# Optimization experiments

Measured on AMD Instinct MI355X. Metric: run time of the kernel, lower is better.

## Reference

```python
import jax, jax.numpy as jnp
import numpy as np

N_NODES = 50000
N_EDGES = 262144
N_OCP = 32768
N_GRAPHS = 64
H = 128          # hidden_size
F_IN = 128       # node feature dim (== H for the stub GNN)
N_LABELS = 10


def _lin(key, fan_in, fan_out):
    return jax.random.normal(key, (fan_in, fan_out), jnp.float32) * (1.0 / float(np.sqrt(fan_in)))


def setup_inputs() -> dict:
    key = jax.random.key(0)
    ks = jax.random.split(key, 16)
    x = jax.random.normal(ks[0], (N_NODES, F_IN), jnp.float32)
    edge_index = jax.random.randint(ks[1], (2, N_EDGES), 0, N_NODES)
    batch_vec = jnp.sort(jax.random.randint(ks[2], (N_NODES,), 0, N_GRAPHS))
    y = jax.random.randint(ks[3], (N_GRAPHS,), 0, N_LABELS)
    params = {
        # stub GNN (get_node_reps): one GCN-style layer
        'W_self': _lin(ks[4], F_IN, H),
        'W_nbr': _lin(ks[5], F_IN, H),
        'b_gnn': jnp.zeros((H,), jnp.float32),
        # edge_action_rep_generator: Linear(2H,4H) ELU Linear(4H,2H) ELU Linear(2H,H)
        'Wr1': _lin(ks[6], 2 * H, 4 * H), 'br1': jnp.zeros((4 * H,), jnp.float32),
        'Wr2': _lin(ks[7], 4 * H, 2 * H), 'br2': jnp.zeros((2 * H,), jnp.float32),
        'Wr3': _lin(ks[8], 2 * H, H),     'br3': jnp.zeros((H,), jnp.float32),
        # edge_action_prob_generator: Linear(H,H) ELU Linear(H,num_labels)
        'Wp1': _lin(ks[9], H, H),         'bp1': jnp.zeros((H,), jnp.float32),
        'Wp2': _lin(ks[10], H, N_LABELS), 'bp2': jnp.zeros((N_LABELS,), jnp.float32),
    }
    return dict(x=x, edge_index=edge_index, batch_vec=batch_vec, y=y, n_ocp=N_OCP, **params)


def reference(x, edge_index, batch_vec, y, n_ocp,
              W_self, W_nbr, b_gnn,
              Wr1, br1, Wr2, br2, Wr3, br3,
              Wp1, bp1, Wp2, bp2):
    N = x.shape[0]
    G = y.shape[0]

    def get_node_reps(ei):
        # stub for self.model.get_node_reps: elu(x @ W_self + A @ (x @ W_nbr))
        msg = x[ei[0]] @ W_nbr                                   # [E', H]
        agg = jax.ops.segment_sum(msg, ei[1], num_segments=N)    # [N, H]
        return jax.nn.elu(x @ W_self + agg + b_gnn)

    ocp_edge_index = edge_index[:, :n_ocp]    # state == True edges
    ava_edge_index = edge_index[:, n_ocp:]    # state == False edges

    ava_node_reps = get_node_reps(edge_index) - get_node_reps(ocp_edge_index)  # [N, H]

    # gather per available edge + concat src/dst reps -> [E_ava, 2H]
    a = jnp.concatenate([ava_node_reps[ava_edge_index[0]],
                         ava_node_reps[ava_edge_index[1]]], axis=1)
    # edge_action_rep_generator
    a = jax.nn.elu(a @ Wr1 + br1)
    a = jax.nn.elu(a @ Wr2 + br2)
    a = a @ Wr3 + br3                                            # [E_ava, H]
    # edge_action_prob_generator
    h = jax.nn.elu(a @ Wp1 + bp1)
    logits = h @ Wp2 + bp2                                       # [E_ava, L]

    seg = batch_vec[ava_edge_index[0]]                           # graph id per ava edge
    y_edge = y[seg]                                              # target label per edge
    sel = jnp.take_along_axis(logits, y_edge[:, None], axis=1)[:, 0]  # gather(1, y)

    # segment-wise softmax over edges of each graph
    mx = jax.ops.segment_max(sel, seg, num_segments=G)
    ex = jnp.exp(sel - mx[seg])
    probs = ex / jax.ops.segment_sum(ex, seg, num_segments=G)[seg]    # [E_ava]

    # scatter_max: per-graph max prob and its argmax edge index
    pmax = jax.ops.segment_max(probs, seg, num_segments=G)            # [G]
    E = probs.shape[0]
    idx = jnp.where(probs == pmax[seg], jnp.arange(E), E)
    added_actions = jax.ops.segment_min(idx, seg, num_segments=G)     # [G]

    return probs, pmax, added_actions
```

## Files before the change

kernel.cpp:

```cpp
#include <hip/hip_runtime.h>

#define NN   50000
#define NNP  50048
#define NE   262144
#define NOCP 32768
#define EAVA (NE - NOCP)
#define NG   64
#define HD   128
#define CAP  48
#define CHNK 32768

typedef _Float16 f16x8 __attribute__((ext_vector_type(8)));
typedef _Float16 f16x2 __attribute__((ext_vector_type(2)));
typedef float f32x4 __attribute__((ext_vector_type(4)));

__device__ __forceinline__ float elu_f(float v) { return v > 0.f ? v : (expf(v) - 1.f); }

__device__ __forceinline__ unsigned fenc(float f) {
  unsigned u = __float_as_uint(f);
  return (u & 0x80000000u) ? ~u : (u | 0x80000000u);
}
__device__ __forceinline__ float fdec(unsigned u) {
  return __uint_as_float((u & 0x80000000u) ? (u & 0x7fffffffu) : ~u);
}

__device__ __forceinline__ void dma16(const void* g, void* l) {
  __builtin_amdgcn_global_load_lds((const __attribute__((address_space(1))) unsigned int*)g,
                                   (__attribute__((address_space(3))) unsigned int*)l,
                                   16, 0, 0);
}

__global__ __launch_bounds__(256) void zero_i(int* __restrict__ p, int n) {
  for (int i = blockIdx.x * 256 + threadIdx.x; i < n; i += gridDim.x * 256) p[i] = 0;
}

__global__ void init_small(unsigned* mx_enc, float* denom, unsigned* pmax_enc, int* amin) {
  int t = threadIdx.x;
  if (t < NG) { mx_enc[t] = 0u; denom[t] = 0.f; pmax_enc[t] = 0u; amin[t] = EAVA; }
}

__global__ __launch_bounds__(256) void zero_tails(_Float16* __restrict__ base) {
  int t = blockIdx.x * 256 + threadIdx.x;
  if (t >= 6 * 768) return;
  int arr = t / 768, off = t % 768;
  f16x8 z = {};
  *(f16x8*)(base + (size_t)arr * NNP * HD + (size_t)NN * HD + (size_t)off * 8) = z;
}

__global__ __launch_bounds__(256) void bucket_kernel(const int* __restrict__ ei,
    int* __restrict__ cnt, int* __restrict__ bucket) {
  int e = blockIdx.x * 256 + threadIdx.x;
  if (e >= NE) return;
  int dst = ei[NE + e];
  int src = ei[e];
  int slot = atomicAdd(&cnt[dst], 1);
  if (slot < CAP)
    bucket[(size_t)dst * CAP + slot] = (int)((unsigned)src | (e < NOCP ? 0x80000000u : 0u));
}

__global__ __launch_bounds__(256) void gather_kernel(const float* __restrict__ x,
    const int* __restrict__ cnt, const int* __restrict__ bucket,
    _Float16* __restrict__ xsah, _Float16* __restrict__ xsal,
    _Float16* __restrict__ xsoh, _Float16* __restrict__ xsol) {
  int n = blockIdx.x * 4 + (threadIdx.x >> 6);
  if (n >= NN) return;
  int lane = threadIdx.x & 63;
  int c = cnt[n];
  if (c > CAP) c = CAP;
  float2 aall = make_float2(0.f, 0.f), aocp = aall;
  const int* bk = bucket + (size_t)n * CAP;
  for (int i0 = 0; i0 < c; i0 += 4) {
    int4 pk = *(const int4*)(bk + i0);
    bool m1 = (i0 + 1 < c), m2 = (i0 + 2 < c), m3 = (i0 + 3 < c);
    int r0 = pk.x & 0x7fffffff;
    int r1 = m1 ? (pk.y & 0x7fffffff) : 0;
    int r2 = m2 ? (pk.z & 0x7fffffff) : 0;
    int r3 = m3 ? (pk.w & 0x7fffffff) : 0;
    float2 v0 = *(const float2*)(x + (size_t)r0 * HD + lane * 2);
    float2 v1 = *(const float2*)(x + (size_t)r1 * HD + lane * 2);
    float2 v2 = *(const float2*)(x + (size_t)r2 * HD + lane * 2);
    float2 v3 = *(const float2*)(x + (size_t)r3 * HD + lane * 2);
    aall.x += v0.x; aall.y += v0.y;
    if (pk.x < 0) { aocp.x += v0.x; aocp.y += v0.y; }
    if (m1) { aall.x += v1.x; aall.y += v1.y; if (pk.y < 0) { aocp.x += v1.x; aocp.y += v1.y; } }
    if (m2) { aall.x += v2.x; aall.y += v2.y; if (pk.z < 0) { aocp.x += v2.x; aocp.y += v2.y; } }
    if (m3) { aall.x += v3.x; aall.y += v3.y; if (pk.w < 0) { aocp.x += v3.x; aocp.y += v3.y; } }
  }
  size_t o = (size_t)n * HD + lane * 2;
  _Float16 h0 = (_Float16)aall.x, h1 = (_Float16)aall.y;
  *(f16x2*)(xsah + o) = (f16x2){h0, h1};
  *(f16x2*)(xsal + o) = (f16x2){(_Float16)(aall.x - (float)h0), (_Float16)(aall.y - (float)h1)};
  _Float16 g0 = (_Float16)aocp.x, g1 = (_Float16)aocp.y;
  *(f16x2*)(xsoh + o) = (f16x2){g0, g1};
  *(f16x2*)(xsol + o) = (f16x2){(_Float16)(aocp.x - (float)g0), (_Float16)(aocp.y - (float)g1)};
}

__global__ __launch_bounds__(256) void split_x(const float* __restrict__ r,
    _Float16* __restrict__ rh, _Float16* __restrict__ rl) {
  int t = blockIdx.x * 256 + threadIdx.x;
  if (t >= NN * HD / 8) return;
  const float4* p = (const float4*)(r + (size_t)t * 8);
  float4 v0 = p[0], v1 = p[1];
  float vv[8] = {v0.x, v0.y, v0.z, v0.w, v1.x, v1.y, v1.z, v1.w};
  f16x8 hv, lv;
#pragma unroll
  for (int j = 0; j < 8; ++j) {
    _Float16 hh = (_Float16)vv[j];
    hv[j] = hh;
    lv[j] = (_Float16)(vv[j] - (float)hh);
  }
  *(f16x8*)(rh + (size_t)t * 8) = hv;
  *(f16x8*)(rl + (size_t)t * 8) = lv;
}

__global__ void pack_w2(const float* __restrict__ Wself, const float* __restrict__ Wnbr,
    _Float16* __restrict__ oh, _Float16* __restrict__ ol) {
  int chunk = blockIdx.x;
  int lane = threadIdx.x;
  int ns = chunk & 7, kt = chunk >> 3;
  int n = ns * 16 + (lane & 15);
  int k0 = kt * 32 + (lane >> 4) * 8;
  f16x8 hv, lv;
#pragma unroll
  for (int j = 0; j < 8; ++j) {
    int k = k0 + j;
    float v = (k < 128) ? Wself[(size_t)k * 128 + n] : Wnbr[(size_t)(k - 128) * 128 + n];
    _Float16 hh = (_Float16)v;
    hv[j] = hh;
    lv[j] = (_Float16)(v - (float)hh);
  }
  *(f16x8*)(oh + (size_t)chunk * 512 + lane * 8) = hv;
  *(f16x8*)(ol + (size_t)chunk * 512 + lane * 8) = lv;
}

__global__ void pack_w(const float* __restrict__ W, int K, int N,
    _Float16* __restrict__ oh, _Float16* __restrict__ ol) {
  int chunk = blockIdx.x;
  int lane = threadIdx.x;
  int NS = N >> 4;
  int ns = chunk % NS, kt = chunk / NS;
  int n = ns * 16 + (lane & 15);
  int k0 = kt * 32 + (lane >> 4) * 8;
  f16x8 hv, lv;
#pragma unroll
  for (int j = 0; j < 8; ++j) {
    float v = W[(size_t)(k0 + j) * N + n];
    _Float16 hh = (_Float16)v;
    hv[j] = hh;
    lv[j] = (_Float16)(v - (float)hh);
  }
  *(f16x8*)(oh + (size_t)chunk * 512 + lane * 8) = hv;
  *(f16x8*)(ol + (size_t)chunk * 512 + lane * 8) = lv;
}

__global__ void w34_kernel(const float* __restrict__ Wr3, const float* __restrict__ Wp1,
    const float* __restrict__ br3, const float* __restrict__ bp1,
    float* __restrict__ W34, float* __restrict__ b34) {
  int i = blockIdx.x, j = threadIdx.x;
  float s = 0.f;
  for (int k = 0; k < 128; ++k) s += Wr3[i * 128 + k] * Wp1[k * 128 + j];
  W34[i * 128 + j] = s;
  if (i == 0) {
    float t = bp1[j];
    for (int k = 0; k < 128; ++k) t += br3[k] * Wp1[k * 128 + j];
    b34[j] = t;
  }
}

template <int KT, int NS_B, int AMODE, int KT_NEXT>
__global__ __launch_bounds__(256) void gemm_ab(
    const _Float16* __restrict__ Ah, const _Float16* __restrict__ Al,
    const int* __restrict__ idx0, const int* __restrict__ idx1,
    const _Float16* __restrict__ Bh, const _Float16* __restrict__ Bl,
    const float* __restrict__ bias,
    _Float16* __restrict__ Oh, _Float16* __restrict__ Ol) {
  __shared__ char smem[49152] __attribute__((aligned(16)));
  float* sC = (float*)smem;

  const int tid = threadIdx.x;
  const int w = tid >> 6, lane = tid & 63;
  const int l16 = lane & 15, g16 = lane >> 4;
  const int bm = blockIdx.x * 128, bn = blockIdx.y * 64;
  const int w2r = w >> 1, w2c = w & 1;
  const int bmT = bm >> 4, bnS = bn >> 4;

  f32x4 acc[4][2];
#pragma unroll
  for (int i = 0; i < 4; ++i)
#pragma unroll
    for (int j = 0; j < 2; ++j) acc[i][j] = (f32x4)0.f;

  int i0a = 0, i0b = 0, i1a = 0, i1b = 0;
  if constexpr (AMODE == 1) {
    int rr0 = bm + w * 32 + l16;
    i0a = idx0[rr0]; i0b = idx0[rr0 + 16];
    i1a = idx1[rr0]; i1b = idx1[rr0 + 16];
  }

  auto STAGE = [&](int kt, int buf) {
    char* base = smem + buf * 24576;
    if constexpr (AMODE == 0) {
#pragma unroll
      for (int s = 0; s < 2; ++s) {
        int msub = w * 2 + s;
        size_t ch = (size_t)(bmT + msub) * KT + kt;
        dma16((const char*)Ah + ch * 1024 + lane * 16, base + msub * 1024);
        dma16((const char*)Al + ch * 1024 + lane * 16, base + 8192 + msub * 1024);
      }
    } else {
      int col = (kt & 3) * 32 + g16 * 8;
      int r0 = (kt < 4) ? i0a : i1a;
      int r1 = (kt < 4) ? i0b : i1b;
      dma16(Ah + (size_t)r0 * HD + col, base + (w * 2) * 1024);
      dma16(Al + (size_t)r0 * HD + col, base + 8192 + (w * 2) * 1024);
      dma16(Ah + (size_t)r1 * HD + col, base + (w * 2 + 1) * 1024);
      dma16(Al + (size_t)r1 * HD + col, base + 8192 + (w * 2 + 1) * 1024);
    }
    size_t chb = (size_t)kt * NS_B + bnS + w;
    dma16((const char*)Bh + chb * 1024 + lane * 16, base + 16384 + w * 1024);
    dma16((const char*)Bl + chb * 1024 + lane * 16, base + 20480 + w * 1024);
  };

  auto COMPUTE = [&](int buf) {
    const _Float16* sAh = (const _Float16*)(smem + buf * 24576);
    const _Float16* sAl = (const _Float16*)(smem + buf * 24576 + 8192);
    const _Float16* sBh = (const _Float16*)(smem + buf * 24576 + 16384);
    const _Float16* sBl = (const _Float16*)(smem + buf * 24576 + 20480);
    f16x8 ah[4], al[4];
#pragma unroll
    for (int mi = 0; mi < 4; ++mi) {
      ah[mi] = *(const f16x8*)(sAh + (w2r * 4 + mi) * 512 + lane * 8);
      al[mi] = *(const f16x8*)(sAl + (w2r * 4 + mi) * 512 + lane * 8);
    }
#pragma unroll
    for (int ni = 0; ni < 2; ++ni) {
      f16x8 bh = *(const f16x8*)(sBh + (w2c * 2 + ni) * 512 + lane * 8);
      f16x8 bl = *(const f16x8*)(sBl + (w2c * 2 + ni) * 512 + lane * 8);
#pragma unroll
      for (int mi = 0; mi < 4; ++mi) {
        acc[mi][ni] = __builtin_amdgcn_mfma_f32_16x16x32_f16(ah[mi], bh, acc[mi][ni], 0, 0, 0);
        acc[mi][ni] = __builtin_amdgcn_mfma_f32_16x16x32_f16(al[mi], bh, acc[mi][ni], 0, 0, 0);
        acc[mi][ni] = __builtin_amdgcn_mfma_f32_16x16x32_f16(ah[mi], bl, acc[mi][ni], 0, 0, 0);
      }
    }
  };

  STAGE(0, 0);
  __builtin_amdgcn_s_waitcnt(0);
  __syncthreads();
  for (int kt = 0; kt < KT; kt += 2) {
    STAGE(kt + 1, 1);
    COMPUTE(0);
    __builtin_amdgcn_s_waitcnt(0);
    __syncthreads();
    if (kt + 2 < KT) STAGE(kt + 2, 0);
    COMPUTE(1);
    __builtin_amdgcn_s_waitcnt(0);
    __syncthreads();
  }

#pragma unroll
  for (int ni = 0; ni < 2; ++ni) {
    int colL = (w2c * 2 + ni) * 16 + l16;
    float bv = bias[bn + colL];
#pragma unroll
    for (int mi = 0; mi < 4; ++mi) {
      int rowb = w2r * 64 + mi * 16 + g16 * 4;
#pragma unroll
      for (int r = 0; r < 4; ++r)
        sC[(rowb + r) * 68 + colL] = elu_f(acc[mi][ni][r] + bv);
    }
  }
  __syncthreads();
  const int bnT32 = bn >> 5;
#pragma unroll
  for (int c = 0; c < 4; ++c) {
    int chunkid = w * 4 + c;
    int msub = chunkid >> 1, ktl = chunkid & 1;
    int m = msub * 16 + l16;
    int cb = ktl * 32 + g16 * 8;
    f16x8 hv, lv;
#pragma unroll
    for (int j = 0; j < 8; ++j) {
      float v = sC[m * 68 + cb + j];
      _Float16 hh = (_Float16)v;
      hv[j] = hh;
      lv[j] = (_Float16)(v - (float)hh);
    }
    size_t gchunk = (size_t)(bmT + msub) * KT_NEXT + (bnT32 + ktl);
    *(f16x8*)((char*)Oh + gchunk * 1024 + lane * 16) = hv;
    *(f16x8*)((char*)Ol + gchunk * 1024 + lane * 16) = lv;
  }
}

__global__ __launch_bounds__(64) void reps_direct(
    const _Float16* __restrict__ xh, const _Float16* __restrict__ xl,
    const _Float16* __restrict__ xsah, const _Float16* __restrict__ xsal,
    const _Float16* __restrict__ xsoh, const _Float16* __restrict__ xsol,
    const _Float16* __restrict__ Wsh, const _Float16* __restrict__ Wsl,
    const float* __restrict__ bias,
    _Float16* __restrict__ Oh, _Float16* __restrict__ Ol) {
  __shared__ float sC[64][68];
  const int lane = threadIdx.x;
  const int mt = blockIdx.x, nt = blockIdx.y;
  const int bm = mt * 64, bn = nt * 64;
  const int l16 = lane & 15, g16 = lane >> 4;

  f32x4 acc1[4][4], acc2[4][4];
#pragma unroll
  for (int i = 0; i < 4; ++i)
#pragma unroll
    for (int j = 0; j < 4; ++j) acc1[i][j] = (f32x4)0.f;

  auto CP3 = [&](f32x4 (*acc)[4], const f16x8* ah, const f16x8* al,
                 const f16x8* bh, const f16x8* bl) {
#pragma unroll
    for (int ni = 0; ni < 4; ++ni)
#pragma unroll
      for (int mi = 0; mi < 4; ++mi) {
        acc[mi][ni] = __builtin_amdgcn_mfma_f32_16x16x32_f16(ah[mi], bh[ni], acc[mi][ni], 0, 0, 0);
        acc[mi][ni] = __builtin_amdgcn_mfma_f32_16x16x32_f16(al[mi], bh[ni], acc[mi][ni], 0, 0, 0);
        acc[mi][ni] = __builtin_amdgcn_mfma_f32_16x16x32_f16(ah[mi], bl[ni], acc[mi][ni], 0, 0, 0);
      }
  };

#pragma unroll
  for (int kt = 0; kt < 4; ++kt) {
    f16x8 ah[4], al[4], bh[4], bl[4];
#pragma unroll
    for (int mi = 0; mi < 4; ++mi) {
      size_t off = (size_t)(bm + mi * 16 + l16) * HD + kt * 32 + g16 * 8;
      ah[mi] = *(const f16x8*)(xh + off);
      al[mi] = *(const f16x8*)(xl + off);
    }
#pragma unroll
    for (int ni = 0; ni < 4; ++ni) {
      size_t ch = (size_t)kt * 8 + nt * 4 + ni;
      bh[ni] = *(const f16x8*)(Wsh + ch * 512 + lane * 8);
      bl[ni] = *(const f16x8*)(Wsl + ch * 512 + lane * 8);
    }
    CP3(acc1, ah, al, bh, bl);
  }
#pragma unroll
  for (int i = 0; i < 4; ++i)
#pragma unroll
    for (int j = 0; j < 4; ++j) acc2[i][j] = acc1[i][j];

#pragma unroll
  for (int kt = 0; kt < 4; ++kt) {
    f16x8 aah[4], aal[4], aoh[4], aol[4], bh[4], bl[4];
#pragma unroll
    for (int mi = 0; mi < 4; ++mi) {
      size_t off = (size_t)(bm + mi * 16 + l16) * HD + kt * 32 + g16 * 8;
      aah[mi] = *(const f16x8*)(xsah + off);
      aal[mi] = *(const f16x8*)(xsal + off);
      aoh[mi] = *(const f16x8*)(xsoh + off);
      aol[mi] = *(const f16x8*)(xsol + off);
    }
#pragma unroll
    for (int ni = 0; ni < 4; ++ni) {
      size_t ch = (size_t)(kt + 4) * 8 + nt * 4 + ni;
      bh[ni] = *(const f16x8*)(Wsh + ch * 512 + lane * 8);
      bl[ni] = *(const f16x8*)(Wsl + ch * 512 + lane * 8);
    }
    CP3(acc1, aah, aal, bh, bl);
    CP3(acc2, aoh, aol, bh, bl);
  }

#pragma unroll
  for (int ni = 0; ni < 4; ++ni) {
    int colL = ni * 16 + l16;
    float bv = bias[bn + colL];
#pragma unroll
    for (int mi = 0; mi < 4; ++mi) {
      int rowb = mi * 16 + g16 * 4;
#pragma unroll
      for (int r = 0; r < 4; ++r)
        sC[rowb + r][colL] = elu_f(acc1[mi][ni][r] + bv) - elu_f(acc2[mi][ni][r] + bv);
    }
  }
  __syncthreads();
#pragma unroll
  for (int c = 0; c < 8; ++c) {
    int msub = c >> 1, ktl = c & 1;
    int m = msub * 16 + l16;
    int cb = ktl * 32 + g16 * 8;
    int grow = bm + m;
    if (grow < NN) {
      f16x8 hv, lv;
#pragma unroll
      for (int j = 0; j < 8; ++j) {
        float v = sC[m][cb + j];
        _Float16 hh = (_Float16)v;
        hv[j] = hh;
        lv[j] = (_Float16)(v - (float)hh);
      }
      *(f16x8*)(Oh + (size_t)grow * HD + bn + cb) = hv;
      *(f16x8*)(Ol + (size_t)grow * HD + bn + cb) = lv;
    }
  }
}

__global__ __launch_bounds__(256) void gemm3_sel(
    const _Float16* __restrict__ Ah, const _Float16* __restrict__ Al,
    const _Float16* __restrict__ Bh, const _Float16* __restrict__ Bl,
    const float* __restrict__ b34,
    const int* __restrict__ ei, const int* __restrict__ batchv, const int* __restrict__ yv,
    const float* __restrict__ Wp2, const float* __restrict__ bp2,
    float* __restrict__ sel, int* __restrict__ seg, int co) {
  __shared__ char smem[49152] __attribute__((aligned(16)));
  const int tid = threadIdx.x;
  const int w = tid >> 6, lane = tid & 63;
  const int l16 = lane & 15, g16 = lane >> 4;
  const int mt = blockIdx.x;

  f32x4 acc[8];
#pragma unroll
  for (int j = 0; j < 8; ++j) acc[j] = (f32x4)0.f;

  auto STAGE = [&](int kt, int buf) {
    char* base = smem + buf * 24576;
    size_t ch = (size_t)(mt * 4 + w) * 8 + kt;
    dma16((const char*)Ah + ch * 1024 + lane * 16, base + w * 1024);
    dma16((const char*)Al + ch * 1024 + lane * 16, base + 4096 + w * 1024);
#pragma unroll
    for (int s = 0; s < 2; ++s) {
      int nsub = w * 2 + s;
      size_t chb = (size_t)kt * 8 + nsub;
      dma16((const char*)Bh + chb * 1024 + lane * 16, base + 8192 + nsub * 1024);
      dma16((const char*)Bl + chb * 1024 + lane * 16, base + 16384 + nsub * 1024);
    }
  };

  auto COMPUTE = [&](int buf) {
    const _Float16* sAh = (const _Float16*)(smem + buf * 24576);
    const _Float16* sAl = (const _Float16*)(smem + buf * 24576 + 4096);
    const _Float16* sBh = (const _Float16*)(smem + buf * 24576 + 8192);
    const _Float16* sBl = (const _Float16*)(smem + buf * 24576 + 16384);
    f16x8 ah = *(const f16x8*)(sAh + w * 512 + lane * 8);
    f16x8 al = *(const f16x8*)(sAl + w * 512 + lane * 8);
#pragma unroll
    for (int ni = 0; ni < 8; ++ni) {
      f16x8 bh = *(const f16x8*)(sBh + ni * 512 + lane * 8);
      f16x8 bl = *(const f16x8*)(sBl + ni * 512 + lane * 8);
      acc[ni] = __builtin_amdgcn_mfma_f32_16x16x32_f16(ah, bh, acc[ni], 0, 0, 0);
      acc[ni] = __builtin_amdgcn_mfma_f32_16x16x32_f16(al, bh, acc[ni], 0, 0, 0);
      acc[ni] = __builtin_amdgcn_mfma_f32_16x16x32_f16(ah, bl, acc[ni], 0, 0, 0);
    }
  };

  STAGE(0, 0);
  __builtin_amdgcn_s_waitcnt(0);
  __syncthreads();
  for (int kt = 0; kt < 8; kt += 2) {
    STAGE(kt + 1, 1);
    COMPUTE(0);
    __builtin_amdgcn_s_waitcnt(0);
    __syncthreads();
    if (kt + 2 < 8) STAGE(kt + 2, 0);
    COMPUTE(1);
    __builtin_amdgcn_s_waitcnt(0);
    __syncthreads();
  }

  float bb[8];
#pragma unroll
  for (int ni = 0; ni < 8; ++ni) bb[ni] = b34[ni * 16 + l16];

#pragma unroll
  for (int rr = 0; rr < 4; ++rr) {
    int row = w * 16 + g16 * 4 + rr;
    int e = co + mt * 64 + row;
    int s = ei[NOCP + e];
    int gg = batchv[s];
    int c = yv[gg];
    float a = 0.f;
#pragma unroll
    for (int ni = 0; ni < 8; ++ni)
      a += elu_f(acc[ni][rr] + bb[ni]) * Wp2[(ni * 16 + l16) * 10 + c];
    a += __shfl_xor(a, 1);
    a += __shfl_xor(a, 2);
    a += __shfl_xor(a, 4);
    a += __shfl_xor(a, 8);
    if (l16 == 0) { sel[e] = a + bp2[c]; seg[e] = gg; }
  }
}

__global__ __launch_bounds__(256) void segmax_sel(const float* __restrict__ sel,
    const int* __restrict__ seg, unsigned* __restrict__ mx_enc) {
  __shared__ unsigned sm[NG];
  int tid = threadIdx.x;
  if (tid < NG) sm[tid] = 0u;
  __syncthreads();
  for (int i = blockIdx.x * blockDim.x + tid; i < EAVA; i += gridDim.x * blockDim.x)
    atomicMax(&sm[seg[i]], fenc(sel[i]));
  __syncthreads();
  if (tid < NG) atomicMax(&mx_enc[tid], sm[tid]);
}

__global__ __launch_bounds__(256) void exden_kernel(const float* __restrict__ sel,
    const int* __restrict__ seg, const unsigned* __restrict__ mx_enc,
    float* __restrict__ denom, float* __restrict__ out_probs) {
  __shared__ float sd[NG];
  __shared__ float smx[NG];
  int tid = threadIdx.x;
  if (tid < NG) { smx[tid] = fdec(mx_enc[tid]); sd[tid] = 0.f; }
  __syncthreads();
  for (int i = blockIdx.x * blockDim.x + tid; i < EAVA; i += gridDim.x * blockDim.x) {
    int g = seg[i];
    float ex = expf(sel[i] - smx[g]);
    out_probs[i] = ex;
    atomicAdd(&sd[g], ex);
  }
  __syncthreads();
  if (tid < NG) atomicAdd(&denom[tid], sd[tid]);
}

__global__ __launch_bounds__(256) void probpmax_kernel(const int* __restrict__ seg,
    const float* __restrict__ denom, float* __restrict__ out_probs,
    unsigned* __restrict__ pmax_enc) {
  __shared__ float sden[NG];
  __shared__ unsigned sp[NG];
  int tid = threadIdx.x;
  if (tid < NG) { sden[tid] = denom[tid]; sp[tid] = 0u; }
  __syncthreads();
  for (int i = blockIdx.x * blockDim.x + tid; i < EAVA; i += gridDim.x * blockDim.x) {
    int g = seg[i];
    float p = out_probs[i] / sden[g];
    out_probs[i] = p;
    atomicMax(&sp[g], fenc(p));
  }
  __syncthreads();
  if (tid < NG) atomicMax(&pmax_enc[tid], sp[tid]);
}

__global__ __launch_bounds__(256) void argmin_kernel(const int* __restrict__ seg,
    const float* __restrict__ out_probs, const unsigned* __restrict__ pmax_enc,
    int* __restrict__ amin) {
  __shared__ float spm[NG];
  __shared__ int sa[NG];
  int tid = threadIdx.x;
  if (tid < NG) { spm[tid] = fdec(pmax_enc[tid]); sa[tid] = EAVA; }
  __syncthreads();
  for (int i = blockIdx.x * blockDim.x + tid; i < EAVA; i += gridDim.x * blockDim.x) {
    int g = seg[i];
    if (out_probs[i] == spm[g]) atomicMin(&sa[g], i);
  }
  __syncthreads();
  if (tid < NG) atomicMin(&amin[tid], sa[tid]);
}

__global__ void finalize_kernel(const unsigned* __restrict__ pmax_enc,
    const int* __restrict__ amin, float* __restrict__ out) {
  int g = threadIdx.x;
  if (g < NG) {
    out[EAVA + g] = fdec(pmax_enc[g]);
    out[EAVA + NG + g] = (float)amin[g];
  }
}

extern "C" void kernel_launch(void* const* d_in, const int* in_sizes, int n_in,
                              void* d_out, int out_size, void* d_ws, size_t ws_size,
                              hipStream_t stream) {
  const float* x      = (const float*)d_in[0];
  const int*   ei     = (const int*)d_in[1];
  const int*   batchv = (const int*)d_in[2];
  const int*   yv     = (const int*)d_in[3];
  const float* Wself = (const float*)d_in[5];
  const float* Wnbr  = (const float*)d_in[6];
  const float* bgnn  = (const float*)d_in[7];
  const float* Wr1   = (const float*)d_in[8];
  const float* br1   = (const float*)d_in[9];
  const float* Wr2   = (const float*)d_in[10];
  const float* br2   = (const float*)d_in[11];
  const float* Wr3   = (const float*)d_in[12];
  const float* br3   = (const float*)d_in[13];
  const float* Wp1   = (const float*)d_in[14];
  const float* bp1   = (const float*)d_in[15];
  const float* Wp2   = (const float*)d_in[16];
  const float* bp2   = (const float*)d_in[17];
  float* out = (float*)d_out;

  char* wp = (char*)d_ws;
  auto alloc = [&](size_t bytes) -> char* {
    char* p = wp;
    wp += (bytes + 255) & ~(size_t)255;
    return p;
  };
  _Float16* xsplit = (_Float16*)alloc((size_t)6 * NNP * HD * 2);
  _Float16* xh   = xsplit + (size_t)0 * NNP * HD;
  _Float16* xl   = xsplit + (size_t)1 * NNP * HD;
  _Float16* xsah = xsplit + (size_t)2 * NNP * HD;
  _Float16* xsal = xsplit + (size_t)3 * NNP * HD;
  _Float16* xsoh = xsplit + (size_t)4 * NNP * HD;
  _Float16* xsol = xsplit + (size_t)5 * NNP * HD;
  _Float16*  reps_h   = (_Float16*)alloc((size_t)NN * HD * 2);
  _Float16*  reps_l   = (_Float16*)alloc((size_t)NN * HD * 2);
  int*       cnt      = (int*)alloc((size_t)NN * 4);
  int*       bucket   = (int*)alloc((size_t)NN * CAP * 4);
  float*     sel      = (float*)alloc((size_t)EAVA * 4);
  int*       seg      = (int*)alloc((size_t)EAVA * 4);
  unsigned*  mx_enc   = (unsigned*)alloc(NG * 4);
  float*     denom    = (float*)alloc(NG * 4);
  unsigned*  pmax_enc = (unsigned*)alloc(NG * 4);
  int*       amin     = (int*)alloc(NG * 4);
  _Float16*  Wsh  = (_Float16*)alloc((size_t)64 * 1024);
  _Float16*  Wsl  = (_Float16*)alloc((size_t)64 * 1024);
  _Float16*  Wr1h = (_Float16*)alloc((size_t)8 * 32 * 1024);
  _Float16*  Wr1l = (_Float16*)alloc((size_t)8 * 32 * 1024);
  _Float16*  Wr2h = (_Float16*)alloc((size_t)16 * 16 * 1024);
  _Float16*  Wr2l = (_Float16*)alloc((size_t)16 * 16 * 1024);
  float*     W34  = (float*)alloc((size_t)256 * 128 * 4);
  float*     b34  = (float*)alloc(128 * 4);
  _Float16*  W34h = (_Float16*)alloc((size_t)8 * 8 * 1024);
  _Float16*  W34l = (_Float16*)alloc((size_t)8 * 8 * 1024);
  _Float16*  b1h = (_Float16*)alloc((size_t)(CHNK / 16) * 16 * 1024);
  _Float16*  b1l = (_Float16*)alloc((size_t)(CHNK / 16) * 16 * 1024);
  _Float16*  b2h = (_Float16*)alloc((size_t)(CHNK / 16) * 8 * 1024);
  _Float16*  b2l = (_Float16*)alloc((size_t)(CHNK / 16) * 8 * 1024);
  (void)ws_size;

  zero_i<<<64, 256, 0, stream>>>(cnt, NN);
  init_small<<<1, 64, 0, stream>>>(mx_enc, denom, pmax_enc, amin);
  zero_tails<<<18, 256, 0, stream>>>(xsplit);
  bucket_kernel<<<NE / 256, 256, 0, stream>>>(ei, cnt, bucket);
  gather_kernel<<<(NN + 3) / 4, 256, 0, stream>>>(x, cnt, bucket, xsah, xsal, xsoh, xsol);
  split_x<<<(NN * HD / 8 + 255) / 256, 256, 0, stream>>>(x, xh, xl);
  pack_w2<<<64, 64, 0, stream>>>(Wself, Wnbr, Wsh, Wsl);
  reps_direct<<<dim3(NNP / 64, 2), 64, 0, stream>>>(xh, xl, xsah, xsal, xsoh, xsol, Wsh, Wsl,
                                                    bgnn, reps_h, reps_l);
  w34_kernel<<<256, 128, 0, stream>>>(Wr3, Wp1, br3, bp1, W34, b34);
  pack_w<<<8 * 32, 64, 0, stream>>>(Wr1, 256, 512, Wr1h, Wr1l);
  pack_w<<<16 * 16, 64, 0, stream>>>(Wr2, 512, 256, Wr2h, Wr2l);
  pack_w<<<8 * 8, 64, 0, stream>>>(W34, 256, 128, W34h, W34l);

  for (int c = 0; c < 7; ++c) {
    int co = c * CHNK;
    gemm_ab<8, 32, 1, 16><<<dim3(CHNK / 128, 8), 256, 0, stream>>>(
        reps_h, reps_l, ei + NOCP + co, ei + NE + NOCP + co, Wr1h, Wr1l, br1, b1h, b1l);
    gemm_ab<16, 16, 0, 8><<<dim3(CHNK / 128, 4), 256, 0, stream>>>(
        b1h, b1l, nullptr, nullptr, Wr2h, Wr2l, br2, b2h, b2l);
    gemm3_sel<<<CHNK / 64, 256, 0, stream>>>(
        b2h, b2l, W34h, W34l, b34, ei, batchv, yv, Wp2, bp2, sel, seg, co);
  }

  segmax_sel<<<112, 256, 0, stream>>>(sel, seg, mx_enc);
  exden_kernel<<<112, 256, 0, stream>>>(sel, seg, mx_enc, denom, out);
  probpmax_kernel<<<112, 256, 0, stream>>>(seg, denom, out, pmax_enc);
  argmin_kernel<<<112, 256, 0, stream>>>(seg, out, pmax_enc, amin);
  finalize_kernel<<<1, 64, 0, stream>>>(pmax_enc, amin, out);
}
```

Baseline: 966.8 us.

## Triple-buffer GEMM LDS staging with partial vmcnt waits and swap grid axes

The GEMM kernels move from a double-buffered loop that drains all loads (waitcnt 0) before every compute step to a three-stage ring buffer. Loads run two k-tiles ahead and the code waits only on the older tile using vmcnt thresholds. The grid axes are also swapped so that blocks sharing the same M rows (the gathered A tiles) launch next to each other, which should improve cache reuse. The trade-off is 72KB of LDS per block instead of 48KB, which can lower occupancy, and the hard-coded vmcnt counts must exactly match the number of loads issued per stage.

```diff
diff --git a/kernel.cpp b/kernel.cpp
--- a/kernel.cpp
+++ b/kernel.cpp
@@ -13,6 +13,10 @@
 typedef _Float16 f16x8 __attribute__((ext_vector_type(8)));
 typedef _Float16 f16x2 __attribute__((ext_vector_type(2)));
 typedef float f32x4 __attribute__((ext_vector_type(4)));
+
+#define WAITVM12() asm volatile("s_waitcnt vmcnt(12)" ::: "memory")
+#define WAITVM6()  asm volatile("s_waitcnt vmcnt(6)" ::: "memory")
+#define WAITVM0()  asm volatile("s_waitcnt vmcnt(0)" ::: "memory")
 
 __device__ __forceinline__ float elu_f(float v) { return v > 0.f ? v : (expf(v) - 1.f); }
 
@@ -174,13 +178,13 @@
     const _Float16* __restrict__ Bh, const _Float16* __restrict__ Bl,
     const float* __restrict__ bias,
     _Float16* __restrict__ Oh, _Float16* __restrict__ Ol) {
-  __shared__ char smem[49152] __attribute__((aligned(16)));
+  __shared__ char smem[73728] __attribute__((aligned(16)));
   float* sC = (float*)smem;
 
   const int tid = threadIdx.x;
   const int w = tid >> 6, lane = tid & 63;
   const int l16 = lane & 15, g16 = lane >> 4;
-  const int bm = blockIdx.x * 128, bn = blockIdx.y * 64;
+  const int bm = blockIdx.y * 128, bn = blockIdx.x * 64;
   const int w2r = w >> 1, w2c = w & 1;
   const int bmT = bm >> 4, bnS = bn >> 4;
 
@@ -246,17 +250,16 @@
   };
 
   STAGE(0, 0);
-  __builtin_amdgcn_s_waitcnt(0);
-  __syncthreads();
-  for (int kt = 0; kt < KT; kt += 2) {
-    STAGE(kt + 1, 1);
-    COMPUTE(0);
-    __builtin_amdgcn_s_waitcnt(0);
-    __syncthreads();
-    if (kt + 2 < KT) STAGE(kt + 2, 0);
-    COMPUTE(1);
-    __builtin_amdgcn_s_waitcnt(0);
-    __syncthreads();
+  STAGE(1, 1);
+#pragma unroll
+  for (int kt = 0; kt < KT; ++kt) {
+    if (kt + 2 < KT) STAGE(kt + 2, (kt + 2) % 3);
+    if (kt < KT - 2) WAITVM12();
+    else if (kt == KT - 2) WAITVM6();
+    else WAITVM0();
+    __builtin_amdgcn_s_barrier();
+    COMPUTE(kt % 3);
+    __builtin_amdgcn_s_barrier();
   }
 
 #pragma unroll
@@ -408,7 +411,7 @@
     const int* __restrict__ ei, const int* __restrict__ batchv, const int* __restrict__ yv,
     const float* __restrict__ Wp2, const float* __restrict__ bp2,
     float* __restrict__ sel, int* __restrict__ seg, int co) {
-  __shared__ char smem[49152] __attribute__((aligned(16)));
+  __shared__ char smem[73728] __attribute__((aligned(16)));
   const int tid = threadIdx.x;
   const int w = tid >> 6, lane = tid & 63;
   const int l16 = lane & 15, g16 = lane >> 4;
@@ -450,17 +453,16 @@
   };
 
   STAGE(0, 0);
-  __builtin_amdgcn_s_waitcnt(0);
-  __syncthreads();
-  for (int kt = 0; kt < 8; kt += 2) {
-    STAGE(kt + 1, 1);
-    COMPUTE(0);
-    __builtin_amdgcn_s_waitcnt(0);
-    __syncthreads();
-    if (kt + 2 < 8) STAGE(kt + 2, 0);
-    COMPUTE(1);
-    __builtin_amdgcn_s_waitcnt(0);
-    __syncthreads();
+  STAGE(1, 1);
+#pragma unroll
+  for (int kt = 0; kt < 8; ++kt) {
+    if (kt + 2 < 8) STAGE(kt + 2, (kt + 2) % 3);
+    if (kt < 6) WAITVM12();
+    else if (kt == 6) WAITVM6();
+    else WAITVM0();
+    __builtin_amdgcn_s_barrier();
+    COMPUTE(kt % 3);
+    __builtin_amdgcn_s_barrier();
   }
 
   float bb[8];
@@ -636,9 +638,9 @@
 
   for (int c = 0; c < 7; ++c) {
     int co = c * CHNK;
-    gemm_ab<8, 32, 1, 16><<<dim3(CHNK / 128, 8), 256, 0, stream>>>(
+    gemm_ab<8, 32, 1, 16><<<dim3(8, CHNK / 128), 256, 0, stream>>>(
         reps_h, reps_l, ei + NOCP + co, ei + NE + NOCP + co, Wr1h, Wr1l, br1, b1h, b1l);
-    gemm_ab<16, 16, 0, 8><<<dim3(CHNK / 128, 4), 256, 0, stream>>>(
+    gemm_ab<16, 16, 0, 8><<<dim3(4, CHNK / 128), 256, 0, stream>>>(
         b1h, b1l, nullptr, nullptr, Wr2h, Wr2l, br2, b2h, b2l);
     gemm3_sel<<<CHNK / 64, 256, 0, stream>>>(
         b2h, b2l, W34h, W34l, b34, ei, batchv, yv, Wp2, bp2, sel, seg, co);
```

After: 1.058 ms. 9.5% more time.
